# Optimization experiments

Measured on AMD Instinct MI355X. Metric: run time of the kernel, lower is better.

The kernel has to match this reference:

```python
import jax, jax.numpy as jnp
import numpy as np

DIM = 512
HEADS = 8
DIM_HEAD = 64
NUM_MEM_KV = 4
H = W = 128


def setup_inputs() -> dict:
    key = jax.random.key(0)
    k1, k2, k3, k4 = jax.random.split(key, 4)
    return {
        "x": jax.random.normal(k1, (DIM, H, W), dtype=jnp.float32),
        "norm1_gamma": jnp.zeros((DIM, 1, 1), dtype=jnp.float32),
        "qkv_w": jax.random.normal(k2, (3 * HEADS * DIM_HEAD, DIM), dtype=jnp.float32) * (DIM ** -0.5),
        "mem_kv": jax.random.normal(k3, (2, HEADS, DIM_HEAD, NUM_MEM_KV), dtype=jnp.float32),
        "conv_w": jax.random.normal(k4, (DIM, HEADS * DIM_HEAD), dtype=jnp.float32) * ((HEADS * DIM_HEAD) ** -0.5),
        "conv_b": jnp.zeros((DIM,), dtype=jnp.float32),
        "norm2_gamma": jnp.zeros((DIM, 1, 1), dtype=jnp.float32),
    }


def rms_norm(x, gamma, dim):
    # x: (c, h, w); L2 norm over channel axis, rescale by sqrt(dim)*(gamma+1)
    n = jnp.linalg.norm(x, ord=2, axis=0)  # (h, w)
    return x / n * (gamma + 1.0) * (dim ** 0.5)


def reference(x, norm1_gamma, qkv_w, mem_kv, conv_w, conv_b, norm2_gamma):
    c, h, w = x.shape
    scale = DIM_HEAD ** -0.5
    xn = rms_norm(x, norm1_gamma, DIM)
    # 1x1 conv == channel matmul
    qkv = jnp.einsum('oc,cxy->oxy', qkv_w, xn)  # (3*hidden, h, w)
    q, k, v = jnp.split(qkv, 3, axis=0)
    def to_heads(t):
        return t.reshape(HEADS, DIM_HEAD, h * w)  # (H, d, n)
    q, k, v = to_heads(q), to_heads(k), to_heads(v)
    mk, mv = mem_kv[0], mem_kv[1]  # (H, d, m)
    k = jnp.concatenate([mk, k], axis=-1)
    v = jnp.concatenate([mv, v], axis=-1)
    q = jax.nn.softmax(q, axis=-2) * scale  # softmax over feature dim d
    k = jax.nn.softmax(k, axis=-1)          # softmax over sequence dim n
    context = jnp.einsum('hdn,hen->hde', k, v)  # (H, d, e)
    out = jnp.einsum('hde,hdn->hen', context, q)  # (H, e, n)
    out = out.reshape(HEADS * DIM_HEAD, h, w)
    out = jnp.einsum('oc,cxy->oxy', conv_w, out) + conv_b[:, None, None]
    return rms_norm(out, norm2_gamma, DIM)
```

## Files before the change

kernel.cpp:

```cpp
#include <hip/hip_runtime.h>
#include <hip/hip_bf16.h>
#include <cstdint>


typedef unsigned short u16;
typedef unsigned int   u32;
typedef short bf16x8 __attribute__((ext_vector_type(8)));
typedef float f32x4  __attribute__((ext_vector_type(4)));

#define HW    16384
#define CDIM  512
#define SQRTD 22.627416997969522f

#define WAITV0 asm volatile("s_waitcnt vmcnt(0)" ::: "memory")
#define WAITL0 asm volatile("s_waitcnt lgkmcnt(0)" ::: "memory")
#define SCHED0 __builtin_amdgcn_sched_barrier(0)

__device__ __forceinline__ u16 f2bf(float f) {
  u32 x = __builtin_bit_cast(u32, f);
  u32 r = x + 0x7fffu + ((x >> 16) & 1u);
  return (u16)(r >> 16);
}

__device__ __forceinline__ void gload16(const void* g, void* l) {
  __builtin_amdgcn_global_load_lds(
      (const __attribute__((address_space(1))) void*)(uintptr_t)g,
      (__attribute__((address_space(3))) void*)(u32)(uintptr_t)l,
      16, 0, 0);
}

__global__ __launch_bounds__(512) void k_pre(const float* __restrict__ x, const float* __restrict__ g1,
                                             const float* __restrict__ qkvw, const float* __restrict__ memkv,
                                             u16* __restrict__ xnt, u16* __restrict__ wbf,
                                             float* __restrict__ den, float* __restrict__ ctx16) {
  __shared__ float tl[512 * 68];
  __shared__ float ssp[8][64];
  __shared__ float rs[64];
  __shared__ float gl[512];
  int t = threadIdx.x, l = t & 63, w = t >> 6;
  int b = blockIdx.x;
  int p0 = b * 64;
  #pragma unroll
  for (int i = 0; i < 16; i++) {
    int idx = i * 512 + t;
    int c = idx >> 4, p4 = (idx & 15) * 4;
    float4 v = *(const float4*)(x + (size_t)c * HW + p0 + p4);
    *(float4*)&tl[c * 68 + p4] = v;
  }
  if (t < 512) gl[t] = 1.0f + g1[t];
  {
    float4 z = make_float4(0.f, 0.f, 0.f, 0.f);
    *(float4*)(ctx16 + (size_t)b * 2048 + t * 4) = z;
  }
  __syncthreads();
  {
    float s = 0.f;
    #pragma unroll
    for (int c = 0; c < 64; c++) {
      float v = tl[(w * 64 + c) * 68 + l];
      s += v * v;
    }
    ssp[w][l] = s;
  }
  __syncthreads();
  if (t < 64) {
    float s = 0.f;
    #pragma unroll
    for (int j = 0; j < 8; j++) s += ssp[j][t];
    rs[t] = SQRTD * rsqrtf(s);
  }
  __syncthreads();
  #pragma unroll
  for (int i = 0; i < 8; i++) {
    int c0 = (i * 8 + w) * 8;
    float sp = rs[l];
    u32 pk[4];
    #pragma unroll
    for (int j = 0; j < 4; j++) {
      float a = tl[(c0 + 2 * j) * 68 + l] * sp * gl[c0 + 2 * j];
      float bq = tl[(c0 + 2 * j + 1) * 68 + l] * sp * gl[c0 + 2 * j + 1];
      pk[j] = (u32)f2bf(a) | ((u32)f2bf(bq) << 16);
    }
    *(uint4*)&xnt[(size_t)(p0 + l) * CDIM + c0] = make_uint4(pk[0], pk[1], pk[2], pk[3]);
  }
  #pragma unroll
  for (int sweep = 0; sweep < 2; sweep++) {
    int idx = (sweep * 256 * 512 + b * 512 + t) * 4;
    if (idx < 1536 * 512) {
      float4 v = *(const float4*)(qkvw + idx);
      ushort4 o; o.x = f2bf(v.x); o.y = f2bf(v.y); o.z = f2bf(v.z); o.w = f2bf(v.w);
      *(ushort4*)(wbf + idx) = o;
    }
  }
  if (b == 0 && t < 512) {
    int h = t >> 6, d = t & 63;
    const float* mk = memkv + ((size_t)h * 64 + d) * 4;
    den[t] = __expf(mk[0]) + __expf(mk[1]) + __expf(mk[2]) + __expf(mk[3]);
  }
}

__global__ __launch_bounds__(256, 2) void k_gemm1(const u16* __restrict__ A, const u16* __restrict__ Bt,
                                                  u16* __restrict__ qT, float* __restrict__ den,
                                                  float* __restrict__ ctx16) {
  const int K = CDIM;
  __shared__ u16 As[2][128 * 64], Bs[2][128 * 64];
  __shared__ float dred[2][64];
  int t = threadIdx.x;
  int lane = t & 63, w = t >> 6;
  int lq = lane >> 4, lr = lane & 15;
  int wg = blockIdx.x;
  int gt = (wg & 7) * 192 + (wg >> 3);
  int bn = gt / 12, bm = gt % 12;
  int wm = (w >> 1) * 64, wn = (w & 1) * 64;
  int h = bm - 4;
  int rb01 = (bm < 4) ? bm * 128 : 512 + h * 64;
  int rb23 = (bm < 4) ? bm * 128 : 960 + h * 64;
  f32x4 acc[4][4] = {};
  const u16* Bbase = Bt + (size_t)bn * 128 * K;

  auto STAGE_A = [&](int buf, int kt) {
    #pragma unroll
    for (int i = 0; i < 4; i++) {
      int s = i * 256 + t;
      int row = s >> 3, slot = (s & 7) ^ (row & 7);
      int rb = (i < 2) ? rb01 : rb23;
      gload16(A + (size_t)(rb + row) * K + kt * 64 + slot * 8, &As[buf][(i * 256 + (w << 6)) * 8]);
    }
  };
  auto STAGE_B = [&](int buf, int kt) {
    #pragma unroll
    for (int i = 0; i < 4; i++) {
      int s = i * 256 + t;
      int row = s >> 3, slot = (s & 7) ^ (row & 7);
      gload16(Bbase + (size_t)row * K + kt * 64 + slot * 8, &Bs[buf][(i * 256 + (w << 6)) * 8]);
    }
  };
  auto FRAGS = [&](int buf, int kk, bf16x8* af, bf16x8* bv) {
    #pragma unroll
    for (int mi = 0; mi < 4; mi++) {
      int row = wm + mi * 16 + lr;
      int slot = ((kk << 2) + lq) ^ (row & 7);
      af[mi] = *(const bf16x8*)&As[buf][row * 64 + slot * 8];
    }
    #pragma unroll
    for (int nj = 0; nj < 4; nj++) {
      int row = wn + nj * 16 + lr;
      int slot = ((kk << 2) + lq) ^ (row & 7);
      bv[nj] = *(const bf16x8*)&Bs[buf][row * 64 + slot * 8];
    }
  };

  STAGE_A(0, 0);
  STAGE_B(0, 0);
  WAITV0;
  __builtin_amdgcn_s_barrier();
  SCHED0;
  for (int kt = 0; kt < 8; kt++) {
    int buf = kt & 1;
    bf16x8 af0[4], bv0[4], af1[4], bv1[4];
    FRAGS(buf, 0, af0, bv0);
    if (kt < 7) STAGE_A(buf ^ 1, kt + 1);
    WAITL0;
    SCHED0;
    __builtin_amdgcn_s_setprio(1);
    #pragma unroll
    for (int mi = 0; mi < 4; mi++)
      #pragma unroll
      for (int nj = 0; nj < 4; nj++)
        acc[mi][nj] = __builtin_amdgcn_mfma_f32_16x16x32_bf16(af0[mi], bv0[nj], acc[mi][nj], 0, 0, 0);
    __builtin_amdgcn_s_setprio(0);
    FRAGS(buf, 1, af1, bv1);
    if (kt < 7) STAGE_B(buf ^ 1, kt + 1);
    WAITL0;
    SCHED0;
    __builtin_amdgcn_s_setprio(1);
    #pragma unroll
    for (int mi = 0; mi < 4; mi++)
      #pragma unroll
      for (int nj = 0; nj < 4; nj++)
        acc[mi][nj] = __builtin_amdgcn_mfma_f32_16x16x32_bf16(af1[mi], bv1[nj], acc[mi][nj], 0, 0, 0);
    __builtin_amdgcn_s_setprio(0);
    if (kt < 7) {
      WAITV0;
      __builtin_amdgcn_s_barrier();
      SCHED0;
    }
  }

  if (bm < 4) {
    __syncthreads();
    u16* As0 = &As[0][0];
    u16* Bs0 = &Bs[0][0];
    #pragma unroll
    for (int nj = 0; nj < 4; nj++) {
      float e[4][4];
      float s = 0.f;
      #pragma unroll
      for (int mi = 0; mi < 4; mi++)
        #pragma unroll
        for (int r = 0; r < 4; r++) { e[mi][r] = __expf(acc[mi][nj][r]); s += e[mi][r]; }
      s += __shfl_xor(s, 16);
      s += __shfl_xor(s, 32);
      float inv = 1.0f / s;
      int pxl = wn + nj * 16 + lr;
      u16* lrow = (pxl < 64 ? As0 : Bs0) + (pxl & 63) * 136;
      #pragma unroll
      for (int mi = 0; mi < 4; mi++) {
        int hdl = wm + mi * 16 + lq * 4;
        ushort4 o;
        o.x = f2bf(e[mi][0] * inv); o.y = f2bf(e[mi][1] * inv);
        o.z = f2bf(e[mi][2] * inv); o.w = f2bf(e[mi][3] * inv);
        *(ushort4*)&lrow[hdl] = o;
      }
    }
    __syncthreads();
    {
      int pxl = t >> 1, half = t & 1;
      const u16* src = (pxl < 64 ? As0 : Bs0) + (pxl & 63) * 136 + half * 64;
      u16* dst = &qT[(size_t)(bn * 128 + pxl) * CDIM + bm * 128 + half * 64];
      #pragma unroll
      for (int j = 0; j < 8; j++) {
        uint4 v = *(const uint4*)(src + j * 8);
        *(uint4*)(dst + j * 8) = v;
      }
    }
  } else {
    __syncthreads();
    u16* Ks = &As[0][0];
    u16* Vs = &Bs[0][0];
    if (w < 2) {
      #pragma unroll
      for (int mi = 0; mi < 4; mi++)
        #pragma unroll
        for (int r = 0; r < 4; r++) {
          int d = mi * 16 + lq * 4 + r;
          float rsum = 0.f;
          #pragma unroll
          for (int nj = 0; nj < 4; nj++) {
            float e = __expf(acc[mi][nj][r]);
            rsum += e;
            int px = wn + nj * 16 + lr;
            Ks[d * 128 + (((px >> 3) ^ (d & 7)) << 3) + (px & 7)] = f2bf(e);
          }
          rsum += __shfl_xor(rsum, 1); rsum += __shfl_xor(rsum, 2);
          rsum += __shfl_xor(rsum, 4); rsum += __shfl_xor(rsum, 8);
          if (lr == 0) dred[w][d] = rsum;
        }
    } else {
      #pragma unroll
      for (int mi = 0; mi < 4; mi++)
        #pragma unroll
        for (int r = 0; r < 4; r++) {
          int e = mi * 16 + lq * 4 + r;
          #pragma unroll
          for (int nj = 0; nj < 4; nj++) {
            int px = wn + nj * 16 + lr;
            Vs[e * 128 + (((px >> 3) ^ (e & 7)) << 3) + (px & 7)] = f2bf(acc[mi][nj][r]);
          }
        }
    }
    __syncthreads();
    if (t < 64) atomicAdd(&den[h * 64 + t], dred[0][t] + dred[1][t]);
    f32x4 c2[4] = {};
    #pragma unroll
    for (int ks = 0; ks < 4; ks++) {
      int ra = w * 16 + lr;
      bf16x8 a = *(const bf16x8*)&Ks[ra * 128 + (((ks * 4 + lq) ^ (ra & 7)) << 3)];
      #pragma unroll
      for (int nj = 0; nj < 4; nj++) {
        int rb2 = nj * 16 + lr;
        bf16x8 b = *(const bf16x8*)&Vs[rb2 * 128 + (((ks * 4 + lq) ^ (rb2 & 7)) << 3)];
        c2[nj] = __builtin_amdgcn_mfma_f32_16x16x32_bf16(a, b, c2[nj], 0, 0, 0);
      }
    }
    float* cp = ctx16 + ((size_t)(bn & 15) * 8 + h) * 4096;
    #pragma unroll
    for (int nj = 0; nj < 4; nj++)
      #pragma unroll
      for (int r = 0; r < 4; r++) {
        int d = w * 16 + lq * 4 + r, e = nj * 16 + lr;
        atomicAdd(&cp[d * 64 + e], c2[nj][r]);
      }
  }
}

__global__ __launch_bounds__(256) void k_fold(const float* __restrict__ convw, const float* __restrict__ ctx16,
                                              const float* __restrict__ den, const float* __restrict__ memkv,
                                              u16* __restrict__ Mbf) {
  __shared__ float cn[64 * 65];
  __shared__ float dn[64];
  __shared__ float emk[256];
  __shared__ float smv[256];
  int t = threadIdx.x;
  int h = blockIdx.x & 7, oc = blockIdx.x >> 3;
  if (t < 64) dn[t] = 0.125f / den[h * 64 + t];
  if (t < 256) emk[t] = __expf(memkv[(size_t)h * 256 + t]);
  if (t < 256) smv[t] = memkv[(size_t)(512 * 4) + h * 256 + t];
  __syncthreads();
  #pragma unroll
  for (int i = 0; i < 16; i++) {
    int idx = i * 256 + t;
    int d = idx >> 6, e = idx & 63;
    float s = emk[d * 4] * smv[e * 4] + emk[d * 4 + 1] * smv[e * 4 + 1]
            + emk[d * 4 + 2] * smv[e * 4 + 2] + emk[d * 4 + 3] * smv[e * 4 + 3];
    #pragma unroll
    for (int rep = 0; rep < 16; rep++) s += ctx16[((size_t)rep * 8 + h) * 4096 + idx];
    cn[d * 65 + e] = s * dn[d];
  }
  __syncthreads();
  int o = oc * 32 + (t >> 3);
  int d0 = (t & 7) * 8;
  float Wr[64];
  const float* wp = convw + (size_t)o * CDIM + h * 64;
  #pragma unroll
  for (int e4 = 0; e4 < 16; e4++) {
    float4 v = *(const float4*)(wp + e4 * 4);
    Wr[e4 * 4] = v.x; Wr[e4 * 4 + 1] = v.y; Wr[e4 * 4 + 2] = v.z; Wr[e4 * 4 + 3] = v.w;
  }
  float outv[8];
  #pragma unroll
  for (int dd = 0; dd < 8; dd++) {
    float a = 0.f;
    #pragma unroll
    for (int e = 0; e < 64; e++) a += Wr[e] * cn[(d0 + dd) * 65 + e];
    outv[dd] = a;
  }
  #pragma unroll
  for (int j = 0; j < 4; j++) {
    u32 v = (u32)f2bf(outv[j * 2]) | ((u32)f2bf(outv[j * 2 + 1]) << 16);
    *(u32*)&Mbf[(size_t)o * CDIM + h * 64 + d0 + j * 2] = v;
  }
}

__global__ __launch_bounds__(512) void k_gemm2(const u16* __restrict__ A, const u16* __restrict__ Bt,
                                               const float* __restrict__ bias, const float* __restrict__ g2,
                                               float* __restrict__ out) {
  __shared__ u16 As[2][512 * 64];
  __shared__ u16 Bs[2][64 * 64];
  __shared__ float css[64];
  int t = threadIdx.x; int lane = t & 63, w = t >> 6, lq = lane >> 4, lr = lane & 15;
  int bn = blockIdx.x;
  if (t < 64) css[t] = 0.f;
  const u16* Bbase = Bt + (size_t)bn * 64 * CDIM;
  f32x4 acc[4][4] = {};

  auto STAGE = [&](int buf, int kt) {
    #pragma unroll
    for (int i = 0; i < 8; i++) {
      int s = i * 512 + t;
      int row = s >> 3, slot = (s & 7) ^ (row & 7);
      gload16(A + (size_t)row * CDIM + kt * 64 + slot * 8, &As[buf][(i * 512 + (w << 6)) * 8]);
    }
    {
      int row = t >> 3, slot = (t & 7) ^ (row & 7);
      gload16(Bbase + (size_t)row * CDIM + kt * 64 + slot * 8, &Bs[buf][(w << 6) * 8]);
    }
  };
  auto FRAGS = [&](int buf, int kk, bf16x8* af, bf16x8* bv) {
    #pragma unroll
    for (int mi = 0; mi < 4; mi++) {
      int row = w * 64 + mi * 16 + lr;
      int slot = ((kk << 2) + lq) ^ (row & 7);
      af[mi] = *(const bf16x8*)&As[buf][row * 64 + slot * 8];
    }
    #pragma unroll
    for (int nj = 0; nj < 4; nj++) {
      int row = nj * 16 + lr;
      int slot = ((kk << 2) + lq) ^ (row & 7);
      bv[nj] = *(const bf16x8*)&Bs[buf][row * 64 + slot * 8];
    }
  };

  STAGE(0, 0);
  WAITV0;
  __builtin_amdgcn_s_barrier();
  SCHED0;
  for (int kt = 0; kt < 8; kt++) {
    int buf = kt & 1;
    bf16x8 af0[4], bv0[4], af1[4], bv1[4];
    FRAGS(buf, 0, af0, bv0);
    if (kt < 7) STAGE(buf ^ 1, kt + 1);
    WAITL0;
    SCHED0;
    __builtin_amdgcn_s_setprio(1);
    #pragma unroll
    for (int mi = 0; mi < 4; mi++)
      #pragma unroll
      for (int nj = 0; nj < 4; nj++)
        acc[mi][nj] = __builtin_amdgcn_mfma_f32_16x16x32_bf16(af0[mi], bv0[nj], acc[mi][nj], 0, 0, 0);
    __builtin_amdgcn_s_setprio(0);
    FRAGS(buf, 1, af1, bv1);
    WAITL0;
    SCHED0;
    __builtin_amdgcn_s_setprio(1);
    #pragma unroll
    for (int mi = 0; mi < 4; mi++)
      #pragma unroll
      for (int nj = 0; nj < 4; nj++)
        acc[mi][nj] = __builtin_amdgcn_mfma_f32_16x16x32_bf16(af1[mi], bv1[nj], acc[mi][nj], 0, 0, 0);
    __builtin_amdgcn_s_setprio(0);
    if (kt < 7) {
      WAITV0;
      __builtin_amdgcn_s_barrier();
      SCHED0;
    }
  }
  __syncthreads();
  float bb[4][4];
  float ps[4] = {0.f, 0.f, 0.f, 0.f};
  #pragma unroll
  for (int mi = 0; mi < 4; mi++)
    #pragma unroll
    for (int r = 0; r < 4; r++) {
      int rowg = w * 64 + mi * 16 + lq * 4 + r;
      bb[mi][r] = bias[rowg];
      #pragma unroll
      for (int nj = 0; nj < 4; nj++) {
        float v = acc[mi][nj][r] + bb[mi][r];
        ps[nj] += v * v;
      }
    }
  #pragma unroll
  for (int nj = 0; nj < 4; nj++) {
    ps[nj] += __shfl_xor(ps[nj], 16);
    ps[nj] += __shfl_xor(ps[nj], 32);
  }
  if (lq == 0) {
    #pragma unroll
    for (int nj = 0; nj < 4; nj++) atomicAdd(&css[nj * 16 + lr], ps[nj]);
  }
  __syncthreads();
  float sc[4];
  #pragma unroll
  for (int nj = 0; nj < 4; nj++) sc[nj] = SQRTD * rsqrtf(css[nj * 16 + lr]);
  #pragma unroll
  for (int mi = 0; mi < 4; mi++)
    #pragma unroll
    for (int r = 0; r < 4; r++) {
      int rowg = w * 64 + mi * 16 + lq * 4 + r;
      float g = 1.0f + g2[rowg];
      #pragma unroll
      for (int nj = 0; nj < 4; nj++) {
        float v = acc[mi][nj][r] + bb[mi][r];
        out[(size_t)rowg * HW + bn * 64 + nj * 16 + lr] = v * sc[nj] * g;
      }
    }
}

extern "C" void kernel_launch(void* const* d_in, const int* in_sizes, int n_in,
                              void* d_out, int out_size, void* d_ws, size_t ws_size,
                              hipStream_t stream) {
  (void)in_sizes; (void)n_in; (void)out_size; (void)ws_size;
  const float* x     = (const float*)d_in[0];
  const float* g1    = (const float*)d_in[1];
  const float* qkvw  = (const float*)d_in[2];
  const float* memkv = (const float*)d_in[3];
  const float* convw = (const float*)d_in[4];
  const float* convb = (const float*)d_in[5];
  const float* g2    = (const float*)d_in[6];
  float* out = (float*)d_out;
  char* ws = (char*)d_ws;

  float* den   = (float*)(ws);
  float* ctx16 = (float*)(ws + 4096);
  u16* Mbf     = (u16*)(ws + 2101248);
  u16* wbf     = (u16*)(ws + 2625536);
  u16* xnt     = (u16*)(ws + 4198400);
  u16* qT      = (u16*)(ws + 20975616);

  k_pre<<<256, 512, 0, stream>>>(x, g1, qkvw, memkv, xnt, wbf, den, ctx16);
  k_gemm1<<<1536, 256, 0, stream>>>(wbf, xnt, qT, den, ctx16);
  k_fold<<<128, 256, 0, stream>>>(convw, ctx16, den, memkv, Mbf);
  k_gemm2<<<256, 512, 0, stream>>>(Mbf, qT, convb, g2, out);
}
```

Measured before the change: 91.05 us.

## Halve k_pre tile per block and write q softmax directly to global

The pre-normalization kernel now handles 32 pixels per block over 512 blocks instead of 64 over 256. This shrinks its shared-memory tile from about 139KB to about 68KB, allowing more resident blocks and spreading work over more CUs, at the cost of narrower 4-byte xnt stores. Separately, the q-softmax epilogue in gemm1 drops its LDS staging and two barriers and writes 8-byte chunks straight to qT. Those direct stores are less coalesced than the previous 16-byte row copies.

```diff
diff --git a/kernel.cpp b/kernel.cpp
--- a/kernel.cpp
+++ b/kernel.cpp
@@ -33,59 +33,53 @@
                                              const float* __restrict__ qkvw, const float* __restrict__ memkv,
                                              u16* __restrict__ xnt, u16* __restrict__ wbf,
                                              float* __restrict__ den, float* __restrict__ ctx16) {
-  __shared__ float tl[512 * 68];
-  __shared__ float ssp[8][64];
-  __shared__ float rs[64];
+  __shared__ float tl[512 * 33];
+  __shared__ float ssp[16][32];
+  __shared__ float rs[32];
   __shared__ float gl[512];
   int t = threadIdx.x, l = t & 63, w = t >> 6;
   int b = blockIdx.x;
-  int p0 = b * 64;
+  int p0 = b * 32;
+  #pragma unroll
+  for (int i = 0; i < 8; i++) {
+    int idx = i * 512 + t;
+    int c = idx >> 3, p4 = (idx & 7) * 4;
+    float4 v = *(const float4*)(x + (size_t)c * HW + p0 + p4);
+    tl[c * 33 + p4] = v.x; tl[c * 33 + p4 + 1] = v.y;
+    tl[c * 33 + p4 + 2] = v.z; tl[c * 33 + p4 + 3] = v.w;
+  }
+  if (t < 512) gl[t] = 1.0f + g1[t];
+  *(float2*)(ctx16 + (size_t)b * 1024 + t * 2) = make_float2(0.f, 0.f);
+  __syncthreads();
+  {
+    int px = l & 31, cg = w * 2 + (l >> 5);
+    float s = 0.f;
+    #pragma unroll
+    for (int c = 0; c < 32; c++) {
+      float v = tl[(cg * 32 + c) * 33 + px];
+      s += v * v;
+    }
+    ssp[cg][px] = s;
+  }
+  __syncthreads();
+  if (t < 32) {
+    float s = 0.f;
+    #pragma unroll
+    for (int j = 0; j < 16; j++) s += ssp[j][t];
+    rs[t] = SQRTD * rsqrtf(s);
+  }
+  __syncthreads();
   #pragma unroll
   for (int i = 0; i < 16; i++) {
     int idx = i * 512 + t;
-    int c = idx >> 4, p4 = (idx & 15) * 4;
-    float4 v = *(const float4*)(x + (size_t)c * HW + p0 + p4);
-    *(float4*)&tl[c * 68 + p4] = v;
-  }
-  if (t < 512) gl[t] = 1.0f + g1[t];
+    int px = idx >> 8, c2 = (idx & 255) * 2;
+    float sp = rs[px];
+    float a = tl[c2 * 33 + px] * sp * gl[c2];
+    float bq = tl[(c2 + 1) * 33 + px] * sp * gl[c2 + 1];
+    *(u32*)&xnt[(size_t)(p0 + px) * CDIM + c2] = (u32)f2bf(a) | ((u32)f2bf(bq) << 16);
+  }
   {
-    float4 z = make_float4(0.f, 0.f, 0.f, 0.f);
-    *(float4*)(ctx16 + (size_t)b * 2048 + t * 4) = z;
-  }
-  __syncthreads();
-  {
-    float s = 0.f;
-    #pragma unroll
-    for (int c = 0; c < 64; c++) {
-      float v = tl[(w * 64 + c) * 68 + l];
-      s += v * v;
-    }
-    ssp[w][l] = s;
-  }
-  __syncthreads();
-  if (t < 64) {
-    float s = 0.f;
-    #pragma unroll
-    for (int j = 0; j < 8; j++) s += ssp[j][t];
-    rs[t] = SQRTD * rsqrtf(s);
-  }
-  __syncthreads();
-  #pragma unroll
-  for (int i = 0; i < 8; i++) {
-    int c0 = (i * 8 + w) * 8;
-    float sp = rs[l];
-    u32 pk[4];
-    #pragma unroll
-    for (int j = 0; j < 4; j++) {
-      float a = tl[(c0 + 2 * j) * 68 + l] * sp * gl[c0 + 2 * j];
-      float bq = tl[(c0 + 2 * j + 1) * 68 + l] * sp * gl[c0 + 2 * j + 1];
-      pk[j] = (u32)f2bf(a) | ((u32)f2bf(bq) << 16);
-    }
-    *(uint4*)&xnt[(size_t)(p0 + l) * CDIM + c0] = make_uint4(pk[0], pk[1], pk[2], pk[3]);
-  }
-  #pragma unroll
-  for (int sweep = 0; sweep < 2; sweep++) {
-    int idx = (sweep * 256 * 512 + b * 512 + t) * 4;
+    int idx = (b * 512 + t) * 4;
     if (idx < 1536 * 512) {
       float4 v = *(const float4*)(qkvw + idx);
       ushort4 o; o.x = f2bf(v.x); o.y = f2bf(v.y); o.z = f2bf(v.z); o.w = f2bf(v.w);
@@ -188,9 +182,7 @@
   }
 
   if (bm < 4) {
-    __syncthreads();
-    u16* As0 = &As[0][0];
-    u16* Bs0 = &Bs[0][0];
+    int cm0 = bm * 128 + wm, cn0 = bn * 128 + wn;
     #pragma unroll
     for (int nj = 0; nj < 4; nj++) {
       float e[4][4];
@@ -202,26 +194,13 @@
       s += __shfl_xor(s, 16);
       s += __shfl_xor(s, 32);
       float inv = 1.0f / s;
-      int pxl = wn + nj * 16 + lr;
-      u16* lrow = (pxl < 64 ? As0 : Bs0) + (pxl & 63) * 136;
+      int col = cn0 + nj * 16 + lr;
       #pragma unroll
       for (int mi = 0; mi < 4; mi++) {
-        int hdl = wm + mi * 16 + lq * 4;
         ushort4 o;
         o.x = f2bf(e[mi][0] * inv); o.y = f2bf(e[mi][1] * inv);
         o.z = f2bf(e[mi][2] * inv); o.w = f2bf(e[mi][3] * inv);
-        *(ushort4*)&lrow[hdl] = o;
-      }
-    }
-    __syncthreads();
-    {
-      int pxl = t >> 1, half = t & 1;
-      const u16* src = (pxl < 64 ? As0 : Bs0) + (pxl & 63) * 136 + half * 64;
-      u16* dst = &qT[(size_t)(bn * 128 + pxl) * CDIM + bm * 128 + half * 64];
-      #pragma unroll
-      for (int j = 0; j < 8; j++) {
-        uint4 v = *(const uint4*)(src + j * 8);
-        *(uint4*)(dst + j * 8) = v;
+        *(ushort4*)&qT[(size_t)col * CDIM + cm0 + mi * 16 + lq * 4] = o;
       }
     }
   } else {
@@ -468,7 +447,7 @@
   u16* xnt     = (u16*)(ws + 4198400);
   u16* qT      = (u16*)(ws + 20975616);
 
-  k_pre<<<256, 512, 0, stream>>>(x, g1, qkvw, memkv, xnt, wbf, den, ctx16);
+  k_pre<<<512, 512, 0, stream>>>(x, g1, qkvw, memkv, xnt, wbf, den, ctx16);
   k_gemm1<<<1536, 256, 0, stream>>>(wbf, xnt, qT, den, ctx16);
   k_fold<<<128, 256, 0, stream>>>(convw, ctx16, den, memkv, Mbf);
   k_gemm2<<<256, 512, 0, stream>>>(Mbf, qT, convb, g2, out);
```

Measured after the change: 84.75 us. -6.9%, faster.
